# Kernel optimization log

Hardware: AMD Instinct MI355X
Metric: run time of the kernel (lower is better)

The kernel has to match this reference:

```python
import jax, jax.numpy as jnp
import numpy as np

BLK = 128            # weight_block_size for w8a16 blockwise dequant
H = 1024             # hidden_size
I = 512              # moe_intermediate_size
E = 64               # n_routed_experts
T = 512              # tokens (seq_len)
K = 6                # num_experts_per_tok
G = 8                # n_group
TG = 3               # topk_group
NSH = 2              # n_shared_experts
I2 = I * NSH         # shared expert intermediate size
ROUTED_SCALE = 2.5
NORM_TOPK = True


def dq(w_int8, scale, blk=BLK):
    """Blockwise w8a16 dequant: w [..., M, N] int8, scale [..., M/blk, N/blk] f32."""
    *lead, M, N = w_int8.shape
    w = w_int8.astype(scale.dtype).reshape(*lead, M // blk, blk, N // blk, blk)
    return (w * scale[..., :, None, :, None]).reshape(*lead, M, N)


def setup_inputs() -> dict:
    key = jax.random.key(0)
    ks = jax.random.split(key, 16)
    ri = lambda k, shp: jax.random.randint(k, shp, -8, 8, dtype=jnp.int8)
    rs = lambda k, shp: jax.random.uniform(k, shp, minval=0.01, maxval=0.03, dtype=jnp.float32)
    return {
        "x": jax.random.normal(ks[0], (T, H), jnp.float32),
        "gate_w": jax.random.normal(ks[1], (E, H), jnp.float32) * 0.02,  # router gate [E,H]
        "wg": ri(ks[2], (E, I, H)),  "sg": rs(ks[3], (E, I // BLK, H // BLK)),
        "wu": ri(ks[4], (E, I, H)),  "su": rs(ks[5], (E, I // BLK, H // BLK)),
        "wd": ri(ks[6], (E, I, H)),  "sd": rs(ks[7], (E, I // BLK, H // BLK)),  # down, transposed layout [I,H]
        "sh_wg": ri(ks[8], (I2, H)),  "sh_sg": rs(ks[9], (I2 // BLK, H // BLK)),
        "sh_wu": ri(ks[10], (I2, H)), "sh_su": rs(ks[11], (I2 // BLK, H // BLK)),
        "sh_wd": ri(ks[12], (I2, H)), "sh_sd": rs(ks[13], (I2 // BLK, H // BLK)),
    }


def _moe(x, gate_w, wg, sg, wu, su, wd, sd, sh_wg, sh_sg, sh_wu, sh_su, sh_wd, sh_sd):
    Tn = x.shape[0]
    # --- router: sigmoid scoring + group-limited top-k ---
    scores = jax.nn.sigmoid(x @ gate_w.T)                       # [T, E]
    gsz = E // G
    group_scores = scores.reshape(Tn, G, gsz).max(axis=-1)      # [T, G]
    _, gidx = jax.lax.top_k(group_scores, TG)                   # [T, TG]
    gmask = jax.nn.one_hot(gidx, G, dtype=scores.dtype).sum(1)  # [T, G]
    emask = jnp.repeat(gmask, gsz, axis=-1)                     # [T, E]
    masked = jnp.where(emask > 0, scores, -jnp.inf)
    w, idx = jax.lax.top_k(masked, K)                           # [T, K]
    if NORM_TOPK:
        w = w / (w.sum(-1, keepdims=True) + 1e-20)
    w = w * ROUTED_SCALE
    # per-token combine weights over experts
    comb = (jax.nn.one_hot(idx, E, dtype=x.dtype) * w[:, :, None]).sum(1)  # [T, E]

    # --- routed experts: dequantized silu-gated MLPs, masked dense combine ---
    Wg, Wu, Wd = dq(wg, sg), dq(wu, su), dq(wd, sd)             # [E, I, H]
    g = jnp.einsum('th,eih->eti', x, Wg)                        # [E, T, I]
    u = jnp.einsum('th,eih->eti', x, Wu)
    hmid = jax.nn.silu(g) * u
    y = jnp.einsum('eti,eih->eth', hmid, Wd)                    # [E, T, H]
    routed = jnp.einsum('eth,te->th', y, comb)                  # [T, H]

    # --- shared experts MLP ---
    Sg, Su, Sd = dq(sh_wg, sh_sg), dq(sh_wu, sh_su), dq(sh_wd, sh_sd)
    shared = (jax.nn.silu(x @ Sg.T) * (x @ Su.T)) @ Sd          # [T, H]
    return routed + shared


def reference(x, gate_w, wg, sg, wu, su, wd, sd, sh_wg, sh_sg, sh_wu, sh_su, sh_wd, sh_sd):
    return _moe(x, gate_w, wg, sg, wu, su, wd, sd,
                sh_wg, sh_sg, sh_wu, sh_su, sh_wd, sh_sd)
```

## Files before the change

### kernel.cpp

```cpp
#include <hip/hip_runtime.h>
#include <math.h>

#define Ttok 512
#define Hd   1024
#define Ne   64
#define Ir   512
#define I2d  1024
#define Kn   6
#define Ngrp 8
#define TGn  3
#define RPAD 7168

typedef __bf16 bf16x8 __attribute__((ext_vector_type(8)));
typedef float f32x4 __attribute__((ext_vector_type(4)));

__device__ __forceinline__ unsigned cvt_pk_bf16(float a, float b) {
  unsigned r;
  asm("v_cvt_pk_bf16_f32 %0, %1, %2" : "=v"(r) : "v"(a), "v"(b));
  return r;
}
__device__ __forceinline__ unsigned short f2bf_rne(float f) {
  unsigned u = __builtin_bit_cast(unsigned, f);
  return (unsigned short)((u + 0x7fffu + ((u >> 16) & 1u)) >> 16);
}
__device__ __forceinline__ float bf2f(unsigned short h) {
  unsigned u = ((unsigned)h) << 16;
  return __builtin_bit_cast(float, u);
}
__device__ __forceinline__ float wred64(float v) {
  #pragma unroll
  for (int m = 32; m >= 1; m >>= 1) v += __shfl_xor(v, m, 64);
  return v;
}

__global__ __launch_bounds__(256) void router_kernel(
    const float* __restrict__ x, const float* __restrict__ gate,
    int* __restrict__ cnt, int* __restrict__ tok, float* __restrict__ wtl)
{
  const int t = blockIdx.x;
  const int lane = threadIdx.x & 63;
  const int wv = threadIdx.x >> 6;
  __shared__ float xs[Hd];
  __shared__ float sc[Ne];
  #pragma unroll
  for (int j = 0; j < 4; ++j) xs[threadIdx.x + 256 * j] = x[(size_t)t * Hd + threadIdx.x + 256 * j];
  __syncthreads();
  #pragma unroll 1
  for (int eo = 0; eo < 16; ++eo) {
    const int e = wv * 16 + eo;
    const float* gr = gate + (size_t)e * Hd;
    float p = 0.f;
    #pragma unroll
    for (int j = 0; j < 16; ++j) p = fmaf(gr[lane + 64 * j], xs[lane + 64 * j], p);
    p = wred64(p);
    if (lane == 0) sc[e] = 1.f / (1.f + expf(-p));
  }
  __syncthreads();
  if (threadIdx.x == 0) {
    float gs[Ngrp];
    #pragma unroll
    for (int g = 0; g < Ngrp; ++g) {
      float m = sc[g * 8];
      #pragma unroll
      for (int j = 1; j < 8; ++j) m = fmaxf(m, sc[g * 8 + j]);
      gs[g] = m;
    }
    unsigned gsel = 0;
    for (int r = 0; r < TGn; ++r) {
      int bg = -1; float bv = -3.4e38f;
      for (int g = 0; g < Ngrp; ++g)
        if (!((gsel >> g) & 1u) && gs[g] > bv) { bv = gs[g]; bg = g; }
      gsel |= 1u << bg;
    }
    int ide[Kn]; float val[Kn];
    unsigned long long taken = 0ull;
    for (int k = 0; k < Kn; ++k) {
      int be = -1; float bv = -3.4e38f;
      for (int e = 0; e < Ne; ++e) {
        if (!((gsel >> (e >> 3)) & 1u)) continue;
        if ((taken >> e) & 1ull) continue;
        if (sc[e] > bv) { bv = sc[e]; be = e; }
      }
      taken |= 1ull << be;
      ide[k] = be; val[k] = bv;
    }
    float s = 0.f;
    for (int k = 0; k < Kn; ++k) s += val[k];
    s += 1e-20f;
    for (int k = 0; k < Kn; ++k) {
      const float w = val[k] / s * 2.5f;
      const int e = ide[k];
      const int slot = atomicAdd(&cnt[e], 1);
      tok[e * Ttok + slot] = t;
      wtl[e * Ttok + slot] = w;
    }
  }
}

__global__ void offs_kernel(const int* __restrict__ cnt, int* __restrict__ offs) {
  if (threadIdx.x == 0 && blockIdx.x == 0) {
    int a = 0;
    for (int e = 0; e < Ne; ++e) { offs[e] = a; a += (cnt[e] + 63) & ~63; }
    offs[Ne] = a;
  }
}

__global__ __launch_bounds__(256) void split_x(
    const float* __restrict__ x, unsigned short* __restrict__ xg)
{
  const int b = blockIdx.x;
  const int lane = threadIdx.x & 63;
  const int q = threadIdx.x >> 6;
  const int r = b * 16 + (lane & 15);
  const int ksub = (lane >> 4) * 8;
  #pragma unroll
  for (int kc = 0; kc < 8; ++kc) {
    const int kblk = q * 8 + kc;
    const float* px = x + (size_t)r * Hd + kblk * 32 + ksub;
    float4 v0 = *(const float4*)(px);
    float4 v1 = *(const float4*)(px + 4);
    uint4 o;
    o.x = cvt_pk_bf16(v0.x, v0.y);
    o.y = cvt_pk_bf16(v0.z, v0.w);
    o.z = cvt_pk_bf16(v1.x, v1.y);
    o.w = cvt_pk_bf16(v1.z, v1.w);
    *(uint4*)(xg + (((size_t)b * 32 + kblk) * 64 + lane) * 8) = o;
  }
}

__global__ __launch_bounds__(256) void gather_x(
    const float* __restrict__ x, const int* __restrict__ tok,
    const int* __restrict__ cnt, const int* __restrict__ offs,
    unsigned short* __restrict__ xg)
{
  const int e = blockIdx.x;
  const int grp = blockIdx.y;
  const int n = cnt[e];
  if (grp * 16 >= n) return;
  const int lane = threadIdx.x & 63;
  const int q = threadIdx.x >> 6;
  const int s = grp * 16 + (lane & 15);
  const bool ok = s < n;
  const int t = ok ? tok[e * Ttok + s] : 0;
  const int g16 = ((Ttok + offs[e]) >> 4) + grp;
  const int ksub = (lane >> 4) * 8;
  #pragma unroll
  for (int kc = 0; kc < 8; ++kc) {
    const int kblk = q * 8 + kc;
    const float* px = x + (size_t)t * Hd + kblk * 32 + ksub;
    float4 v0 = *(const float4*)(px);
    float4 v1 = *(const float4*)(px + 4);
    uint4 o;
    o.x = cvt_pk_bf16(v0.x, v0.y);
    o.y = cvt_pk_bf16(v0.z, v0.w);
    o.z = cvt_pk_bf16(v1.x, v1.y);
    o.w = cvt_pk_bf16(v1.z, v1.w);
    if (ok) *(uint4*)(xg + (((size_t)g16 * 32 + kblk) * 64 + lane) * 8) = o;
  }
}

__global__ __launch_bounds__(256) void gu_mfma(
    const unsigned short* __restrict__ xg,
    const int* __restrict__ wgq, const float* __restrict__ sgs,
    const int* __restrict__ wuq, const float* __restrict__ sus,
    const int* __restrict__ cnt, const int* __restrict__ offs,
    unsigned short* __restrict__ hm, int Idim)
{
  const int e = blockIdx.y;
  const int n = cnt ? cnt[e] : Ttok;
  const int mbase = blockIdx.z * 64;
  if (mbase >= n) return;
  const int lane = threadIdx.x & 63;
  const int wv = threadIdx.x >> 6;
  const int iL = lane & 15;
  const int qk = lane >> 4;
  const int i0 = blockIdx.x * 64;
  const int g16x = ((offs ? (Ttok + offs[e]) : 0) + mbase) >> 4;
  const int g16h = ((offs ? offs[e] : 0) + mbase) >> 4;

  __shared__ char smem[65536];
  char* Ab0 = smem;
  char* Ab1 = smem + 16384;
  char* Bg = smem + 32768 + wv * 8192;
  char* Bu = Bg + 4096;

  const int sRows = Idim >> 7;
  const float* sG = sgs + ((size_t)e * sRows + (i0 >> 7)) * 8;
  const float* sU = sus + ((size_t)e * sRows + (i0 >> 7)) * 8;

  const int jrh = lane >> 5;
  const int kint = (lane & 31) * 4;
  const int* pG = wgq + ((size_t)e * Idim + i0 + wv * 16) * Hd;
  const int* pU = wuq + ((size_t)e * Idim + i0 + wv * 16) * Hd;

  int4 graw[8], uraw[8];
  f32x4 aG[4] = {{0,0,0,0},{0,0,0,0},{0,0,0,0},{0,0,0,0}};
  f32x4 aU[4] = {{0,0,0,0},{0,0,0,0},{0,0,0,0},{0,0,0,0}};

  auto loadB = [&](int kb) {
    #pragma unroll
    for (int j = 0; j < 8; ++j) {
      const size_t off = (size_t)(j * 2 + jrh) * Hd + kb * 128 + kint;
      graw[j] = *(const int4*)(pG + off);
      uraw[j] = *(const int4*)(pU + off);
    }
  };
  auto stageA = [&](int kb, char* dstbuf) {
    const unsigned short* src = xg + (((size_t)(g16x + wv) * 32 + kb * 4) * 64 + lane) * 8;
    char* dst = dstbuf + wv * 4096 + lane * 16;
    uint4 t0 = *(const uint4*)(src);
    uint4 t1 = *(const uint4*)(src + 512);
    uint4 t2 = *(const uint4*)(src + 1024);
    uint4 t3 = *(const uint4*)(src + 1536);
    *(uint4*)(dst) = t0;
    *(uint4*)(dst + 1024) = t1;
    *(uint4*)(dst + 2048) = t2;
    *(uint4*)(dst + 3072) = t3;
  };
  auto cvtWriteB = [&](int kb) {
    const float fg = sG[kb], fu = sU[kb];
    #pragma unroll
    for (int j = 0; j < 8; ++j) {
      const int r = j * 2 + jrh;
      const int w0 = r * 64 + ((kint >> 1) ^ ((r & 7) << 2));
      uint2 gv, uv;
      gv.x = cvt_pk_bf16((float)graw[j].x * fg, (float)graw[j].y * fg);
      gv.y = cvt_pk_bf16((float)graw[j].z * fg, (float)graw[j].w * fg);
      uv.x = cvt_pk_bf16((float)uraw[j].x * fu, (float)uraw[j].y * fu);
      uv.y = cvt_pk_bf16((float)uraw[j].z * fu, (float)uraw[j].w * fu);
      *(uint2*)(Bg + w0 * 4) = gv;
      *(uint2*)(Bu + w0 * 4) = uv;
    }
  };
  auto mfmaStep = [&](char* A) {
    #pragma unroll
    for (int ks = 0; ks < 4; ++ks) {
      const int bw = (iL * 64 + ((ks * 16 + qk * 4) ^ ((iL & 7) << 2))) * 4;
      bf16x8 bg = *(const bf16x8*)(Bg + bw);
      bf16x8 bu = *(const bf16x8*)(Bu + bw);
      #pragma unroll
      for (int mt = 0; mt < 4; ++mt) {
        bf16x8 a = *(const bf16x8*)(A + mt * 4096 + ks * 1024 + lane * 16);
        aG[mt] = __builtin_amdgcn_mfma_f32_16x16x32_bf16(a, bg, aG[mt], 0, 0, 0);
        aU[mt] = __builtin_amdgcn_mfma_f32_16x16x32_bf16(a, bu, aU[mt], 0, 0, 0);
      }
    }
  };

  stageA(0, Ab0);
  loadB(0);
  __syncthreads();
  #pragma unroll 1
  for (int kb = 0; kb < 8; ++kb) {
    cvtWriteB(kb);
    if (kb < 7) {
      stageA(kb + 1, (kb & 1) ? Ab0 : Ab1);
      loadB(kb + 1);
    }
    mfmaStep((kb & 1) ? Ab1 : Ab0);
    __syncthreads();
  }

  float* tile = (float*)(smem + 32768);
  #pragma unroll
  for (int mt = 0; mt < 4; ++mt) {
    #pragma unroll
    for (int j = 0; j < 4; ++j) {
      const float g = aG[mt][j], u = aU[mt][j];
      tile[(mt * 16 + qk * 4 + j) * 68 + wv * 16 + iL] = g / (1.f + expf(-g)) * u;
    }
  }
  __syncthreads();
  const int nkb = Idim >> 5;
  #pragma unroll
  for (int ib = 0; ib < 2; ++ib) {
    const float* srcp = tile + (wv * 16 + iL) * 68 + ib * 32 + qk * 8;
    uint4 ov;
    ov.x = cvt_pk_bf16(srcp[0], srcp[1]);
    ov.y = cvt_pk_bf16(srcp[2], srcp[3]);
    ov.z = cvt_pk_bf16(srcp[4], srcp[5]);
    ov.w = cvt_pk_bf16(srcp[6], srcp[7]);
    *(uint4*)(hm + (((size_t)(g16h + wv) * nkb + (i0 >> 5) + ib) * 64 + lane) * 8) = ov;
  }
}

__global__ __launch_bounds__(256) void down_mfma(
    const unsigned short* __restrict__ hm,
    const int* __restrict__ wdq, const float* __restrict__ sds,
    const int* __restrict__ cnt, const int* __restrict__ offs,
    const int* __restrict__ toks, const float* __restrict__ wtl,
    float* __restrict__ out, int Kd)
{
  const int e = blockIdx.y;
  const int n = cnt ? cnt[e] : Ttok;
  const int mbase = blockIdx.z * 64;
  if (mbase >= n) return;
  const int lane = threadIdx.x & 63;
  const int wv = threadIdx.x >> 6;
  const int hL = lane & 15;
  const int qk = lane >> 4;
  const int h0 = blockIdx.x * 64;
  const int g16a = ((offs ? offs[e] : 0) + mbase) >> 4;

  __shared__ char smem[49152];
  char* Ab0 = smem;
  char* Ab1 = smem + 16384;
  char* Bd = smem + 32768 + wv * 4096;

  const float* sD = sds + ((size_t)e * (Kd >> 7)) * 8 + (h0 >> 7);
  const int kLl = lane >> 2;
  const int hoff = (lane & 3) * 4;
  const int* pW = wdq + (size_t)e * Kd * Hd + h0 + wv * 16 + hoff;
  const int nka = Kd >> 5;

  int4 draw[8];
  f32x4 acc[4] = {{0,0,0,0},{0,0,0,0},{0,0,0,0},{0,0,0,0}};

  auto loadB = [&](int kb) {
    #pragma unroll
    for (int j = 0; j < 8; ++j)
      draw[j] = *(const int4*)(pW + (size_t)(kb * 128 + j * 16 + kLl) * Hd);
  };
  auto stageA = [&](int kb, char* dstbuf) {
    const unsigned short* src = hm + (((size_t)(g16a + wv) * nka + kb * 4) * 64 + lane) * 8;
    char* dst = dstbuf + wv * 4096 + lane * 16;
    uint4 t0 = *(const uint4*)(src);
    uint4 t1 = *(const uint4*)(src + 512);
    uint4 t2 = *(const uint4*)(src + 1024);
    uint4 t3 = *(const uint4*)(src + 1536);
    *(uint4*)(dst) = t0;
    *(uint4*)(dst + 1024) = t1;
    *(uint4*)(dst + 2048) = t2;
    *(uint4*)(dst + 3072) = t3;
  };
  auto cvtWriteB = [&](int kb) {
    const float fd = sD[kb * 8];
    #pragma unroll
    for (int j = 0; j < 8; ++j) {
      const int kL = j * 16 + kLl;
      const int* dv = &draw[j].x;
      #pragma unroll
      for (int c = 0; c < 4; ++c) {
        const int hl = hoff + c;
        const int addr = ((hl * 64 + ((kL >> 1) ^ ((hl & 7) << 2))) << 2) + (kL & 1) * 2;
        *(unsigned short*)(Bd + addr) = f2bf_rne((float)dv[c] * fd);
      }
    }
  };
  auto mfmaStep = [&](char* A) {
    #pragma unroll
    for (int ks = 0; ks < 4; ++ks) {
      bf16x8 b = *(const bf16x8*)(Bd + (hL * 64 + ((ks * 16 + qk * 4) ^ ((hL & 7) << 2))) * 4);
      #pragma unroll
      for (int mt = 0; mt < 4; ++mt) {
        bf16x8 a = *(const bf16x8*)(A + mt * 4096 + ks * 1024 + lane * 16);
        acc[mt] = __builtin_amdgcn_mfma_f32_16x16x32_bf16(a, b, acc[mt], 0, 0, 0);
      }
    }
  };

  const int nKb = Kd >> 7;
  stageA(0, Ab0);
  loadB(0);
  __syncthreads();
  #pragma unroll 1
  for (int kb = 0; kb < nKb; ++kb) {
    cvtWriteB(kb);
    if (kb + 1 < nKb) {
      stageA(kb + 1, (kb & 1) ? Ab0 : Ab1);
      loadB(kb + 1);
    }
    mfmaStep((kb & 1) ? Ab1 : Ab0);
    __syncthreads();
  }

  const int hW = h0 + wv * 16 + hL;
  #pragma unroll
  for (int mt = 0; mt < 4; ++mt) {
    #pragma unroll
    for (int j = 0; j < 4; ++j) {
      const int mr = mbase + mt * 16 + qk * 4 + j;
      if (mr < n) {
        const int t = toks ? toks[e * Ttok + mr] : mr;
        const float wt = wtl ? wtl[e * Ttok + mr] : 1.f;
        atomicAdd(&out[(size_t)t * Hd + hW], wt * acc[mt][j]);
      }
    }
  }
}

extern "C" void kernel_launch(void* const* d_in, const int* in_sizes, int n_in,
                              void* d_out, int out_size, void* d_ws, size_t ws_size,
                              hipStream_t stream)
{
  const float* x    = (const float*)d_in[0];
  const float* gate = (const float*)d_in[1];
  const int*   wg   = (const int*)d_in[2];
  const float* sg   = (const float*)d_in[3];
  const int*   wu   = (const int*)d_in[4];
  const float* su   = (const float*)d_in[5];
  const int*   wd   = (const int*)d_in[6];
  const float* sd   = (const float*)d_in[7];
  const int*   shwg = (const int*)d_in[8];
  const float* shsg = (const float*)d_in[9];
  const int*   shwu = (const int*)d_in[10];
  const float* shsu = (const float*)d_in[11];
  const int*   shwd = (const int*)d_in[12];
  const float* shsd = (const float*)d_in[13];
  float* out = (float*)d_out;

  char* p = (char*)d_ws;
  auto nxt = [&](size_t bytes) { char* r = p; p += (bytes + 255) & ~(size_t)255; return r; };
  int*   cnt  = (int*)nxt(Ne * 4);
  int*   offs = (int*)nxt((Ne + 1) * 4);
  int*   tok  = (int*)nxt((size_t)Ne * Ttok * 4);
  float* wtl  = (float*)nxt((size_t)Ne * Ttok * 4);
  unsigned short* xg = (unsigned short*)nxt((size_t)(Ttok + RPAD) * Hd * 2);
  unsigned short* hr = (unsigned short*)nxt((size_t)RPAD * Ir * 2);
  unsigned short* hs = (unsigned short*)nxt((size_t)Ttok * I2d * 2);

  hipMemsetAsync(cnt, 0, Ne * 4, stream);
  hipMemsetAsync(out, 0, (size_t)out_size * sizeof(float), stream);

  router_kernel<<<Ttok, 256, 0, stream>>>(x, gate, cnt, tok, wtl);
  offs_kernel<<<1, 64, 0, stream>>>(cnt, offs);
  split_x<<<Ttok / 16, 256, 0, stream>>>(x, xg);
  gather_x<<<dim3(Ne, Ttok / 16), 256, 0, stream>>>(x, tok, cnt, offs, xg);

  gu_mfma<<<dim3(Ir / 64, Ne, 8), 256, 0, stream>>>(
      xg, wg, sg, wu, su, cnt, offs, hr, Ir);
  gu_mfma<<<dim3(I2d / 64, 1, 8), 256, 0, stream>>>(
      xg, shwg, shsg, shwu, shsu, nullptr, nullptr, hs, I2d);

  down_mfma<<<dim3(Hd / 64, Ne, 8), 256, 0, stream>>>(
      hr, wd, sd, cnt, offs, tok, wtl, out, Ir);
  down_mfma<<<dim3(Hd / 64, 1, 8), 256, 0, stream>>>(
      hs, shwd, shsd, nullptr, nullptr, nullptr, nullptr, out, I2d);
}
```

Before: 524.5 us.

## Load A fragments directly to registers and widen down-proj tile to 128 columns

Both MFMA kernels stop staging the activation tile through shared memory. Each wave now loads all four M-tiles of A straight into registers and prefetches the next K-block after its MFMAs, which drops the per-iteration __syncthreads and halves LDS use. The down kernel now covers 128 H columns per block with two 16-wide tiles per wave, so the grid is halved and each A load is reused twice. Launch bounds request two blocks per CU. The trade-off is more VGPRs and redundant global A loads across waves, since each of the four waves reads the full 64-row A tile.

```diff
diff --git a/kernel.cpp b/kernel.cpp
--- a/kernel.cpp
+++ b/kernel.cpp
@@ -22,10 +22,6 @@
 __device__ __forceinline__ unsigned short f2bf_rne(float f) {
   unsigned u = __builtin_bit_cast(unsigned, f);
   return (unsigned short)((u + 0x7fffu + ((u >> 16) & 1u)) >> 16);
-}
-__device__ __forceinline__ float bf2f(unsigned short h) {
-  unsigned u = ((unsigned)h) << 16;
-  return __builtin_bit_cast(float, u);
 }
 __device__ __forceinline__ float wred64(float v) {
   #pragma unroll
@@ -159,7 +155,7 @@
   }
 }
 
-__global__ __launch_bounds__(256) void gu_mfma(
+__global__ __launch_bounds__(256, 2) void gu_mfma(
     const unsigned short* __restrict__ xg,
     const int* __restrict__ wgq, const float* __restrict__ sgs,
     const int* __restrict__ wuq, const float* __restrict__ sus,
@@ -178,10 +174,8 @@
   const int g16x = ((offs ? (Ttok + offs[e]) : 0) + mbase) >> 4;
   const int g16h = ((offs ? offs[e] : 0) + mbase) >> 4;
 
-  __shared__ char smem[65536];
-  char* Ab0 = smem;
-  char* Ab1 = smem + 16384;
-  char* Bg = smem + 32768 + wv * 8192;
+  __shared__ char smem[32768];
+  char* Bg = smem + wv * 8192;
   char* Bu = Bg + 4096;
 
   const int sRows = Idim >> 7;
@@ -194,6 +188,7 @@
   const int* pU = wuq + ((size_t)e * Idim + i0 + wv * 16) * Hd;
 
   int4 graw[8], uraw[8];
+  uint4 av[4][4];
   f32x4 aG[4] = {{0,0,0,0},{0,0,0,0},{0,0,0,0},{0,0,0,0}};
   f32x4 aU[4] = {{0,0,0,0},{0,0,0,0},{0,0,0,0},{0,0,0,0}};
 
@@ -205,17 +200,12 @@
       uraw[j] = *(const int4*)(pU + off);
     }
   };
-  auto stageA = [&](int kb, char* dstbuf) {
-    const unsigned short* src = xg + (((size_t)(g16x + wv) * 32 + kb * 4) * 64 + lane) * 8;
-    char* dst = dstbuf + wv * 4096 + lane * 16;
-    uint4 t0 = *(const uint4*)(src);
-    uint4 t1 = *(const uint4*)(src + 512);
-    uint4 t2 = *(const uint4*)(src + 1024);
-    uint4 t3 = *(const uint4*)(src + 1536);
-    *(uint4*)(dst) = t0;
-    *(uint4*)(dst + 1024) = t1;
-    *(uint4*)(dst + 2048) = t2;
-    *(uint4*)(dst + 3072) = t3;
+  auto loadA = [&](int kb) {
+    #pragma unroll
+    for (int mt = 0; mt < 4; ++mt)
+      #pragma unroll
+      for (int ks = 0; ks < 4; ++ks)
+        av[mt][ks] = *(const uint4*)(xg + (((size_t)(g16x + mt) * 32 + kb * 4 + ks) * 64 + lane) * 8);
   };
   auto cvtWriteB = [&](int kb) {
     const float fg = sG[kb], fu = sU[kb];
@@ -232,7 +222,13 @@
       *(uint2*)(Bu + w0 * 4) = uv;
     }
   };
-  auto mfmaStep = [&](char* A) {
+
+  loadB(0);
+  loadA(0);
+  #pragma unroll 1
+  for (int kb = 0; kb < 8; ++kb) {
+    cvtWriteB(kb);
+    if (kb < 7) loadB(kb + 1);
     #pragma unroll
     for (int ks = 0; ks < 4; ++ks) {
       const int bw = (iL * 64 + ((ks * 16 + qk * 4) ^ ((iL & 7) << 2))) * 4;
@@ -240,28 +236,16 @@
       bf16x8 bu = *(const bf16x8*)(Bu + bw);
       #pragma unroll
       for (int mt = 0; mt < 4; ++mt) {
-        bf16x8 a = *(const bf16x8*)(A + mt * 4096 + ks * 1024 + lane * 16);
+        bf16x8 a = __builtin_bit_cast(bf16x8, av[mt][ks]);
         aG[mt] = __builtin_amdgcn_mfma_f32_16x16x32_bf16(a, bg, aG[mt], 0, 0, 0);
         aU[mt] = __builtin_amdgcn_mfma_f32_16x16x32_bf16(a, bu, aU[mt], 0, 0, 0);
       }
     }
-  };
-
-  stageA(0, Ab0);
-  loadB(0);
+    if (kb < 7) loadA(kb + 1);
+  }
+
   __syncthreads();
-  #pragma unroll 1
-  for (int kb = 0; kb < 8; ++kb) {
-    cvtWriteB(kb);
-    if (kb < 7) {
-      stageA(kb + 1, (kb & 1) ? Ab0 : Ab1);
-      loadB(kb + 1);
-    }
-    mfmaStep((kb & 1) ? Ab1 : Ab0);
-    __syncthreads();
-  }
-
-  float* tile = (float*)(smem + 32768);
+  float* tile = (float*)smem;
   #pragma unroll
   for (int mt = 0; mt < 4; ++mt) {
     #pragma unroll
@@ -284,7 +268,7 @@
   }
 }
 
-__global__ __launch_bounds__(256) void down_mfma(
+__global__ __launch_bounds__(256, 2) void down_mfma(
     const unsigned short* __restrict__ hm,
     const int* __restrict__ wdq, const float* __restrict__ sds,
     const int* __restrict__ cnt, const int* __restrict__ offs,
@@ -297,84 +281,76 @@
   if (mbase >= n) return;
   const int lane = threadIdx.x & 63;
   const int wv = threadIdx.x >> 6;
-  const int hL = lane & 15;
+  const int iL = lane & 15;
   const int qk = lane >> 4;
-  const int h0 = blockIdx.x * 64;
+  const int h0 = blockIdx.x * 128;
+  const int hw = h0 + wv * 32;
   const int g16a = ((offs ? offs[e] : 0) + mbase) >> 4;
-
-  __shared__ char smem[49152];
-  char* Ab0 = smem;
-  char* Ab1 = smem + 16384;
-  char* Bd = smem + 32768 + wv * 4096;
-
-  const float* sD = sds + ((size_t)e * (Kd >> 7)) * 8 + (h0 >> 7);
-  const int kLl = lane >> 2;
-  const int hoff = (lane & 3) * 4;
-  const int* pW = wdq + (size_t)e * Kd * Hd + h0 + wv * 16 + hoff;
   const int nka = Kd >> 5;
 
-  int4 draw[8];
-  f32x4 acc[4] = {{0,0,0,0},{0,0,0,0},{0,0,0,0},{0,0,0,0}};
+  __shared__ char smem[32768];
+  char* Bd = smem + wv * 8192;
+
+  const float* sD = sds + (size_t)e * (Kd >> 7) * 8 + (h0 >> 7);
+  const int kj = lane >> 3;
+  const int hc = (lane & 7) * 4;
+  const int* pW = wdq + (size_t)e * Kd * Hd + hw + hc;
+
+  int4 draw[16];
+  uint4 av[4][4];
+  f32x4 acc[4][2] = {{{0,0,0,0},{0,0,0,0}},{{0,0,0,0},{0,0,0,0}},
+                     {{0,0,0,0},{0,0,0,0}},{{0,0,0,0},{0,0,0,0}}};
 
   auto loadB = [&](int kb) {
     #pragma unroll
-    for (int j = 0; j < 8; ++j)
-      draw[j] = *(const int4*)(pW + (size_t)(kb * 128 + j * 16 + kLl) * Hd);
-  };
-  auto stageA = [&](int kb, char* dstbuf) {
-    const unsigned short* src = hm + (((size_t)(g16a + wv) * nka + kb * 4) * 64 + lane) * 8;
-    char* dst = dstbuf + wv * 4096 + lane * 16;
-    uint4 t0 = *(const uint4*)(src);
-    uint4 t1 = *(const uint4*)(src + 512);
-    uint4 t2 = *(const uint4*)(src + 1024);
-    uint4 t3 = *(const uint4*)(src + 1536);
-    *(uint4*)(dst) = t0;
-    *(uint4*)(dst + 1024) = t1;
-    *(uint4*)(dst + 2048) = t2;
-    *(uint4*)(dst + 3072) = t3;
+    for (int j = 0; j < 16; ++j)
+      draw[j] = *(const int4*)(pW + (size_t)(kb * 128 + j * 8 + kj) * Hd);
+  };
+  auto loadA = [&](int kb) {
+    #pragma unroll
+    for (int mt = 0; mt < 4; ++mt)
+      #pragma unroll
+      for (int ks = 0; ks < 4; ++ks)
+        av[mt][ks] = *(const uint4*)(hm + (((size_t)(g16a + mt) * nka + kb * 4 + ks) * 64 + lane) * 8);
   };
   auto cvtWriteB = [&](int kb) {
     const float fd = sD[kb * 8];
     #pragma unroll
-    for (int j = 0; j < 8; ++j) {
-      const int kL = j * 16 + kLl;
+    for (int j = 0; j < 16; ++j) {
+      const int kL = j * 8 + kj;
       const int* dv = &draw[j].x;
       #pragma unroll
       for (int c = 0; c < 4; ++c) {
-        const int hl = hoff + c;
+        const int hl = hc + c;
         const int addr = ((hl * 64 + ((kL >> 1) ^ ((hl & 7) << 2))) << 2) + (kL & 1) * 2;
         *(unsigned short*)(Bd + addr) = f2bf_rne((float)dv[c] * fd);
       }
     }
   };
-  auto mfmaStep = [&](char* A) {
-    #pragma unroll
-    for (int ks = 0; ks < 4; ++ks) {
-      bf16x8 b = *(const bf16x8*)(Bd + (hL * 64 + ((ks * 16 + qk * 4) ^ ((hL & 7) << 2))) * 4);
-      #pragma unroll
-      for (int mt = 0; mt < 4; ++mt) {
-        bf16x8 a = *(const bf16x8*)(A + mt * 4096 + ks * 1024 + lane * 16);
-        acc[mt] = __builtin_amdgcn_mfma_f32_16x16x32_bf16(a, b, acc[mt], 0, 0, 0);
-      }
-    }
-  };
 
   const int nKb = Kd >> 7;
-  stageA(0, Ab0);
   loadB(0);
-  __syncthreads();
+  loadA(0);
   #pragma unroll 1
   for (int kb = 0; kb < nKb; ++kb) {
     cvtWriteB(kb);
-    if (kb + 1 < nKb) {
-      stageA(kb + 1, (kb & 1) ? Ab0 : Ab1);
-      loadB(kb + 1);
-    }
-    mfmaStep((kb & 1) ? Ab1 : Ab0);
-    __syncthreads();
-  }
-
-  const int hW = h0 + wv * 16 + hL;
+    if (kb + 1 < nKb) loadB(kb + 1);
+    #pragma unroll
+    for (int ks = 0; ks < 4; ++ks) {
+      #pragma unroll
+      for (int ht = 0; ht < 2; ++ht) {
+        const int row = ht * 16 + iL;
+        bf16x8 b = *(const bf16x8*)(Bd + (row * 64 + ((ks * 16 + qk * 4) ^ ((row & 7) << 2))) * 4);
+        #pragma unroll
+        for (int mt = 0; mt < 4; ++mt) {
+          bf16x8 a = __builtin_bit_cast(bf16x8, av[mt][ks]);
+          acc[mt][ht] = __builtin_amdgcn_mfma_f32_16x16x32_bf16(a, b, acc[mt][ht], 0, 0, 0);
+        }
+      }
+    }
+    if (kb + 1 < nKb) loadA(kb + 1);
+  }
+
   #pragma unroll
   for (int mt = 0; mt < 4; ++mt) {
     #pragma unroll
@@ -383,7 +359,8 @@
       if (mr < n) {
         const int t = toks ? toks[e * Ttok + mr] : mr;
         const float wt = wtl ? wtl[e * Ttok + mr] : 1.f;
-        atomicAdd(&out[(size_t)t * Hd + hW], wt * acc[mt][j]);
+        atomicAdd(&out[(size_t)t * Hd + hw + iL], wt * acc[mt][0][j]);
+        atomicAdd(&out[(size_t)t * Hd + hw + 16 + iL], wt * acc[mt][1][j]);
       }
     }
   }
@@ -432,8 +409,8 @@
   gu_mfma<<<dim3(I2d / 64, 1, 8), 256, 0, stream>>>(
       xg, shwg, shsg, shwu, shsu, nullptr, nullptr, hs, I2d);
 
-  down_mfma<<<dim3(Hd / 64, Ne, 8), 256, 0, stream>>>(
+  down_mfma<<<dim3(Hd / 128, Ne, 8), 256, 0, stream>>>(
       hr, wd, sd, cnt, offs, tok, wtl, out, Ir);
-  down_mfma<<<dim3(Hd / 64, 1, 8), 256, 0, stream>>>(
+  down_mfma<<<dim3(Hd / 128, 1, 8), 256, 0, stream>>>(
       hs, shwd, shsd, nullptr, nullptr, nullptr, nullptr, out, I2d);
 }
```

Result: no change. 516.1 us (-1.6%).
